# Performance work log

Measured on AMD Instinct MI355X. Metric: run time of the kernel, lower is better.

The kernel has to match this reference:

```python
import jax, jax.numpy as jnp
import numpy as np

TAU = 0.3  # default tau in selectCom_adap
K = 1      # hard-coded K in selectCom_adap

B, C, N, M = 8, 64, 2048, 2048


def setup_inputs() -> dict:
    key = jax.random.key(0)
    k1, k2, k3, k4 = jax.random.split(key, 4)
    return {
        "src_emb": jax.random.normal(k1, (B, C, N), dtype=jnp.float32),
        "tgt_emb": jax.random.normal(k2, (B, C, M), dtype=jnp.float32),
        "src": jax.random.normal(k3, (B, 3, N), dtype=jnp.float32),
        "tgt": jax.random.normal(k4, (B, 3, M), dtype=jnp.float32),
    }


def reference(src_emb, tgt_emb, src, tgt):
    # EPCOR eval path: selectCom_adap + get_sparse_w
    dtype = src_emb.dtype
    Np = src_emb.shape[2]
    Mp = tgt_emb.shape[2]
    tgt_K = int(Mp * TAU)
    src_K = int(Np * TAU)

    inner = jnp.einsum('bcn,bcm->bnm', src_emb, tgt_emb)
    xx = jnp.sum(src_emb * src_emb, axis=1)[:, :, None]   # [B,N,1]
    yy = jnp.sum(tgt_emb * tgt_emb, axis=1)[:, None, :]   # [B,1,M]
    pd = 2.0 * inner - xx - yy                             # [B,N,M]

    # column softmax and tgt outlier mask (smallest tgt_K column mass)
    scoresSoftCol = jax.nn.softmax(pd, axis=2)
    scoresColSum = jnp.sum(scoresSoftCol, axis=1)          # [B,M]
    col_thresh = -jax.lax.top_k(-scoresColSum, tgt_K)[0][:, -1]  # tgt_K-th smallest, [B]
    mask_tgt = (scoresColSum < col_thresh[:, None])[:, None, :]  # [B,1,M]

    # row softmax and src outlier mask (smallest src_K row mass)
    scoresSoftRow = jax.nn.softmax(pd, axis=1)
    scoresRowSum = jnp.sum(scoresSoftRow, axis=2)          # [B,N]
    row_thresh = -jax.lax.top_k(-scoresRowSum, src_K)[0][:, -1]  # [B]
    mask_src = (scoresRowSum < row_thresh[:, None])[:, :, None]  # [B,N,1]

    mask = jnp.logical_or(mask_src, mask_tgt)              # [B,N,M]

    # torch precedence: mask = (mask + scoresSoftCol) < topk  (bool promoted to float)
    topk = jax.lax.top_k(scoresSoftCol, K)[0][..., -1:]    # K-th largest per row, [B,N,1]
    mask = (mask.astype(dtype) + scoresSoftCol) < topk     # [B,N,M]

    w_sparse = jnp.where(mask, jnp.zeros((), dtype), scoresSoftCol)
    colsum = jnp.sum(w_sparse, axis=-1, keepdims=True)
    colsum = jnp.where(colsum < 1e-5, jnp.asarray(1e-5, dtype), colsum)
    src_tgt_weight = w_sparse / colsum                     # row-renormalized sparse weights

    val_sum = jnp.sum(src_tgt_weight, axis=-1, keepdims=True)  # [B,N,1]
    val_sum_inlier = jnp.where(mask_src, jnp.zeros((), dtype), val_sum)[..., 0]  # [B,N]
    src_weight = val_sum_inlier / jnp.sum(val_sum_inlier, axis=-1, keepdims=True)

    # src_corr = tgt @ src_tgt_weight^T : [B,3,M] x [B,N,M] -> [B,3,N]
    src_corr = jnp.einsum('bdm,bnm->bdn', tgt, src_tgt_weight)
    return src_corr, src_weight, mask_src, mask_tgt
```

## Files before the change

### kernel.cpp

```cpp
#include <hip/hip_runtime.h>

#define BB 8
#define CC 64
#define NN 2048
#define MM 2048
#define KSEL 613
#define MT 32
#define MT2 16
#define NT2 16
#define NCH 16

#define OUT_W  (BB * 3 * NN)
#define OUT_MS (OUT_W + BB * NN)
#define OUT_MT (OUT_MS + BB * NN)

typedef __bf16 bf16x8 __attribute__((ext_vector_type(8)));
typedef float f32x4 __attribute__((ext_vector_type(4)));

__global__ __launch_bounds__(256) void sqnorm_k(const float* __restrict__ E,
                                                float* __restrict__ out, int L) {
    int b = blockIdx.y;
    int i = blockIdx.x * 256 + threadIdx.x;
    const float* p = E + (size_t)b * CC * L + i;
    float s = 0.f;
#pragma unroll
    for (int c = 0; c < CC; ++c) { float v = p[(size_t)c * L]; s += v * v; }
    out[b * L + i] = s;
}

__device__ __forceinline__ void build3(const float* sm, int base,
                                       bf16x8& v0, bf16x8& v1, bf16x8& v2) {
#pragma unroll
    for (int j = 0; j < 8; ++j) {
        float a = sm[base + (j << 7)];
        __bf16 h0 = (__bf16)a;
        float f0 = (float)h0;
        float r1 = a - f0;
        __bf16 h1 = (__bf16)r1;
        float f1 = (float)h1;
        float r2 = r1 - f1;
        __bf16 h2 = (__bf16)r2;
        v0[j] = h0; v1[j] = h1; v2[j] = h2;
    }
}

#define GLD_LDS16(gsrc, ldst)                                                        \
    __builtin_amdgcn_global_load_lds(                                                \
        (const __attribute__((address_space(1))) void*)(gsrc),                       \
        (__attribute__((address_space(3))) void*)(ldst), 16, 0, 0)

__global__ __launch_bounds__(256, 2) void gemm_pd_k(const float* __restrict__ A,
                                                    const float* __restrict__ Bm,
                                                    const float* __restrict__ xx,
                                                    const float* __restrict__ yy,
                                                    float* __restrict__ pd,
                                                    float* __restrict__ rpM,
                                                    float* __restrict__ rpS,
                                                    float* __restrict__ cpM,
                                                    float* __restrict__ cpS) {
    __shared__ float As[CC * 128];
    __shared__ float Bs[CC * 128];
    __shared__ float rowm2[2][128], rows2[2][128];
    __shared__ float colm2[2][128], cols2[2][128];
    int b = blockIdx.z;
    int n0 = blockIdx.y << 7;
    int m0 = blockIdx.x << 7;
    int t = threadIdx.x;

    const float* Ab = A + (size_t)b * CC * NN + n0;
    const float* Bb = Bm + (size_t)b * CC * MM + m0;
#pragma unroll
    for (int i = 0; i < 8; ++i) {
        int fi = i * 256 + t;
        int c = fi >> 5, nb = fi & 31;
        GLD_LDS16(Ab + (size_t)c * NN + nb * 4, As + fi * 4);
        GLD_LDS16(Bb + (size_t)c * MM + nb * 4, Bs + fi * 4);
    }
    __syncthreads();

    int lane = t & 63, w = t >> 6;
    int wn = w >> 1, wm = w & 1;
    int g = lane >> 4, q = lane & 15;

    f32x4 acc[4][4] = {};

#pragma unroll
    for (int kc = 0; kc < 2; ++kc) {
        bf16x8 a0[4], a1[4], a2[4];
#pragma unroll
        for (int ng = 0; ng < 4; ++ng)
            build3(As, (kc * 32 + g * 8) * 128 + wn * 64 + ng * 16 + q,
                   a0[ng], a1[ng], a2[ng]);
#pragma unroll
        for (int mg = 0; mg < 4; ++mg) {
            bf16x8 b0, b1, b2;
            build3(Bs, (kc * 32 + g * 8) * 128 + wm * 64 + mg * 16 + q, b0, b1, b2);
#pragma unroll
            for (int ng = 0; ng < 4; ++ng)
                acc[ng][mg] = __builtin_amdgcn_mfma_f32_16x16x32_bf16(a0[ng], b0, acc[ng][mg], 0, 0, 0);
#pragma unroll
            for (int ng = 0; ng < 4; ++ng)
                acc[ng][mg] = __builtin_amdgcn_mfma_f32_16x16x32_bf16(a0[ng], b1, acc[ng][mg], 0, 0, 0);
#pragma unroll
            for (int ng = 0; ng < 4; ++ng)
                acc[ng][mg] = __builtin_amdgcn_mfma_f32_16x16x32_bf16(a1[ng], b0, acc[ng][mg], 0, 0, 0);
#pragma unroll
            for (int ng = 0; ng < 4; ++ng)
                acc[ng][mg] = __builtin_amdgcn_mfma_f32_16x16x32_bf16(a1[ng], b1, acc[ng][mg], 0, 0, 0);
#pragma unroll
            for (int ng = 0; ng < 4; ++ng)
                acc[ng][mg] = __builtin_amdgcn_mfma_f32_16x16x32_bf16(a0[ng], b2, acc[ng][mg], 0, 0, 0);
#pragma unroll
            for (int ng = 0; ng < 4; ++ng)
                acc[ng][mg] = __builtin_amdgcn_mfma_f32_16x16x32_bf16(a2[ng], b0, acc[ng][mg], 0, 0, 0);
        }
    }

    int nbase = n0 + wn * 64;
    int mbase = m0 + wm * 64;
    float xv[4][4];
#pragma unroll
    for (int ng = 0; ng < 4; ++ng)
#pragma unroll
        for (int r = 0; r < 4; ++r)
            xv[ng][r] = xx[b * NN + nbase + ng * 16 + g * 4 + r];
    float yv[4];
#pragma unroll
    for (int mg = 0; mg < 4; ++mg) yv[mg] = yy[b * MM + mbase + mg * 16 + q];

#pragma unroll
    for (int ng = 0; ng < 4; ++ng)
#pragma unroll
        for (int r = 0; r < 4; ++r) {
            float* prow = pd + ((size_t)(b * NN + nbase + ng * 16 + g * 4 + r)) * MM + mbase + q;
#pragma unroll
            for (int mg = 0; mg < 4; ++mg) {
                float o = 2.f * acc[ng][mg][r] - xv[ng][r] - yv[mg];
                acc[ng][mg][r] = o;
                prow[mg * 16] = o;
            }
        }

#pragma unroll
    for (int ng = 0; ng < 4; ++ng)
#pragma unroll
        for (int r = 0; r < 4; ++r) {
            float mx = fmaxf(fmaxf(acc[ng][0][r], acc[ng][1][r]),
                             fmaxf(acc[ng][2][r], acc[ng][3][r]));
#pragma unroll
            for (int d = 1; d < 16; d <<= 1) mx = fmaxf(mx, __shfl_xor(mx, d));
            float s = __expf(acc[ng][0][r] - mx) + __expf(acc[ng][1][r] - mx) +
                      __expf(acc[ng][2][r] - mx) + __expf(acc[ng][3][r] - mx);
#pragma unroll
            for (int d = 1; d < 16; d <<= 1) s += __shfl_xor(s, d);
            if (q == 0) {
                int nl = wn * 64 + ng * 16 + g * 4 + r;
                rowm2[wm][nl] = mx;
                rows2[wm][nl] = s;
            }
        }

#pragma unroll
    for (int mg = 0; mg < 4; ++mg) {
        float cx = -3.4e38f;
#pragma unroll
        for (int ng = 0; ng < 4; ++ng)
#pragma unroll
            for (int r = 0; r < 4; ++r) cx = fmaxf(cx, acc[ng][mg][r]);
        cx = fmaxf(cx, __shfl_xor(cx, 16));
        cx = fmaxf(cx, __shfl_xor(cx, 32));
        float cs = 0.f;
#pragma unroll
        for (int ng = 0; ng < 4; ++ng)
#pragma unroll
            for (int r = 0; r < 4; ++r) cs += __expf(acc[ng][mg][r] - cx);
        cs += __shfl_xor(cs, 16);
        cs += __shfl_xor(cs, 32);
        if (lane < 16) {
            int ml = wm * 64 + mg * 16 + q;
            colm2[wn][ml] = cx;
            cols2[wn][ml] = cs;
        }
    }
    __syncthreads();

    if (t < 128) {
        float ma = rowm2[0][t], mb = rowm2[1][t];
        float M = fmaxf(ma, mb);
        float S = rows2[0][t] * __expf(ma - M) + rows2[1][t] * __expf(mb - M);
        size_t base = ((size_t)(b * MT2 + blockIdx.x)) * NN + n0 + t;
        rpM[base] = M;
        rpS[base] = S;
    } else {
        int m = t - 128;
        float ma = colm2[0][m], mb = colm2[1][m];
        float M = fmaxf(ma, mb);
        float S = cols2[0][m] * __expf(ma - M) + cols2[1][m] * __expf(mb - M);
        size_t base = ((size_t)(b * NT2 + blockIdx.y)) * MM + m0 + m;
        cpM[base] = M;
        cpS[base] = S;
    }
}

__global__ __launch_bounds__(256) void comb_rc_k(const float* __restrict__ rpM,
                                                 const float* __restrict__ rpS,
                                                 const float* __restrict__ cpM,
                                                 const float* __restrict__ cpS,
                                                 float* __restrict__ rowmax,
                                                 float* __restrict__ rowsum,
                                                 float* __restrict__ colmax,
                                                 float* __restrict__ colsum) {
    int b = blockIdx.y, which = blockIdx.z;
    int i = blockIdx.x * 256 + threadIdx.x;
    const float* pM = which ? cpM : rpM;
    const float* pS = which ? cpS : rpS;
    float* oM = which ? colmax : rowmax;
    float* oS = which ? colsum : rowsum;
    float Mv = -3.4e38f;
#pragma unroll
    for (int k = 0; k < 16; ++k) Mv = fmaxf(Mv, pM[(size_t)(b * 16 + k) * 2048 + i]);
    float S = 0.f;
#pragma unroll
    for (int k = 0; k < 16; ++k) {
        size_t o = (size_t)(b * 16 + k) * 2048 + i;
        S += pS[o] * __expf(pM[o] - Mv);
    }
    oM[b * 2048 + i] = Mv;
    oS[b * 2048 + i] = S;
}

__global__ __launch_bounds__(256) void cross_k(const float* __restrict__ pd,
                                               const float* __restrict__ rowmax,
                                               const float* __restrict__ rowsum,
                                               const float* __restrict__ colmax,
                                               const float* __restrict__ colsum,
                                               float* __restrict__ sRowp,
                                               float* __restrict__ sColp) {
    __shared__ float rmx[128], rin[128];
    __shared__ float rowpart[128][65];
    __shared__ float colacc[4][64];
    int b = blockIdx.z, nc = blockIdx.y, mtile = blockIdx.x;
    int m0 = mtile << 6;
    int t = threadIdx.x, mL = t & 63, ng = t >> 6;
    if (t < 128) {
        int n = nc * 128 + t;
        rmx[t] = rowmax[b * NN + n];
        rin[t] = 1.f / rowsum[b * NN + n];
    }
    float cmv = colmax[b * MM + m0 + mL];
    float civ = 1.f / colsum[b * MM + m0 + mL];
    __syncthreads();
    const float* base = pd + ((size_t)(b * NN + nc * 128)) * MM + m0 + mL;
    float scp = 0.f;
#pragma unroll
    for (int i = 0; i < 32; ++i) {
        int nl = (i << 2) + ng;
        float v = base[(size_t)nl * MM];
        scp += __expf(v - rmx[nl]) * rin[nl];
        rowpart[nl][mL] = __expf(v - cmv) * civ;
    }
    colacc[ng][mL] = scp;
    __syncthreads();
    if (t < 128) {
        float s = 0.f;
#pragma unroll
        for (int c = 0; c < 64; ++c) s += rowpart[t][c];
        sRowp[((size_t)(b * MT + mtile)) * NN + nc * 128 + t] = s;
    } else if (t < 192) {
        int m = t - 128;
        sColp[((size_t)(b * NCH + nc)) * MM + m0 + m] =
            colacc[0][m] + colacc[1][m] + colacc[2][m] + colacc[3][m];
    }
}

__global__ __launch_bounds__(256) void comb_s_k(const float* __restrict__ sRowp,
                                                const float* __restrict__ sColp,
                                                float* __restrict__ sRow,
                                                float* __restrict__ sCol) {
    int b = blockIdx.y, which = blockIdx.z;
    int i = blockIdx.x * 256 + threadIdx.x;
    if (!which) {
        float s = 0.f;
#pragma unroll
        for (int k = 0; k < MT; ++k) s += sRowp[(size_t)(b * MT + k) * NN + i];
        sRow[b * NN + i] = s;
    } else {
        float s = 0.f;
#pragma unroll
        for (int k = 0; k < NCH; ++k) s += sColp[(size_t)(b * NCH + k) * MM + i];
        sCol[b * MM + i] = s;
    }
}

__global__ __launch_bounds__(64) void select_k(const float* __restrict__ sRow,
                                               const float* __restrict__ sCol,
                                               float* __restrict__ rth,
                                               float* __restrict__ cth) {
    int kind = blockIdx.x, b = blockIdx.y, t = threadIdx.x;
    const float* vals = (kind == 0) ? (sRow + b * NN) : (sCol + b * MM);
    float v[32];
#pragma unroll
    for (int i = 0; i < 32; ++i) v[i] = vals[t + (i << 6)];
    unsigned lo = 0u, hi = 0x7F800000u;
    while (lo < hi) {
        unsigned mid = lo + ((hi - lo) >> 1);
        float pv = __uint_as_float(mid);
        int c = 0;
#pragma unroll
        for (int i = 0; i < 32; ++i) c += (v[i] <= pv) ? 1 : 0;
#pragma unroll
        for (int off = 32; off > 0; off >>= 1) c += __shfl_down(c, off);
        c = __shfl(c, 0);
        if (c >= KSEL + 1) hi = mid; else lo = mid + 1;
    }
    if (t == 0) { if (kind == 0) rth[b] = __uint_as_float(lo); else cth[b] = __uint_as_float(lo); }
}

__global__ __launch_bounds__(256) void masks_k(const float* __restrict__ sRow,
                                               const float* __restrict__ sCol,
                                               const float* __restrict__ rth,
                                               const float* __restrict__ cth,
                                               float* __restrict__ out) {
    int b = blockIdx.x, t = threadIdx.x;
    float r = rth[b], c = cth[b];
    int cnt = 0;
    bool ms[8];
#pragma unroll
    for (int i = 0; i < 8; ++i) {
        int n = t + (i << 8);
        ms[i] = sRow[b * NN + n] < r;
        out[OUT_MS + b * NN + n] = ms[i] ? 1.f : 0.f;
        out[OUT_MT + b * MM + n] = (sCol[b * MM + n] < c) ? 1.f : 0.f;
        cnt += ms[i] ? 0 : 1;
    }
#pragma unroll
    for (int off = 32; off > 0; off >>= 1) cnt += __shfl_down(cnt, off);
    __shared__ int wcnt[4];
    int wave = t >> 6, lane = t & 63;
    if (lane == 0) wcnt[wave] = cnt;
    __syncthreads();
    float inv = 1.f / (float)(wcnt[0] + wcnt[1] + wcnt[2] + wcnt[3]);
#pragma unroll
    for (int i = 0; i < 8; ++i) {
        int n = t + (i << 8);
        out[OUT_W + b * NN + n] = ms[i] ? 0.f : inv;
    }
}

__global__ __launch_bounds__(256) void corr_k(const float* __restrict__ pd,
                                              const float* __restrict__ rowmax,
                                              const float* __restrict__ rowsum,
                                              const float* __restrict__ sRow,
                                              const float* __restrict__ sCol,
                                              const float* __restrict__ rth,
                                              const float* __restrict__ cth,
                                              const float* __restrict__ tgt,
                                              float* __restrict__ out) {
    int b = blockIdx.y, n = blockIdx.x, t = threadIdx.x;
    const float4* row4 = (const float4*)(pd + ((size_t)b * NN + n) * MM);
    const float4* sc4 = (const float4*)(sCol + b * MM);
    const float4* tg4 = (const float4*)(tgt + (size_t)b * 3 * MM);
    float rmax = rowmax[b * NN + n];
    float rsum = rowsum[b * NN + n];
    float cthv = cth[b];
    bool msrc = sRow[b * NN + n] < rth[b];
    float cs = 0.f, d0 = 0.f, d1 = 0.f, d2 = 0.f;
#pragma unroll
    for (int g = 0; g < 2; ++g) {
        int j = t + (g << 8);
        float p[4], sc[4], t0[4], t1[4], t2[4];
        *(float4*)p = row4[j];
        *(float4*)sc = sc4[j];
        *(float4*)t0 = tg4[j];
        *(float4*)t1 = tg4[j + MM / 4];
        *(float4*)t2 = tg4[j + MM / 2];
#pragma unroll
        for (int c = 0; c < 4; ++c) {
            bool keep = msrc || (sc[c] < cthv) || (p[c] == rmax);
            if (keep) {
                float s = __expf(p[c] - rmax) / rsum;
                cs += s;
                d0 += s * t0[c];
                d1 += s * t1[c];
                d2 += s * t2[c];
            }
        }
    }
#pragma unroll
    for (int off = 32; off > 0; off >>= 1) {
        cs += __shfl_down(cs, off);
        d0 += __shfl_down(d0, off);
        d1 += __shfl_down(d1, off);
        d2 += __shfl_down(d2, off);
    }
    __shared__ float red[4][4];
    int wave = t >> 6, lane = t & 63;
    if (lane == 0) { red[wave][0] = cs; red[wave][1] = d0; red[wave][2] = d1; red[wave][3] = d2; }
    __syncthreads();
    if (t == 0) {
        float cT = red[0][0] + red[1][0] + red[2][0] + red[3][0];
        float e0 = red[0][1] + red[1][1] + red[2][1] + red[3][1];
        float e1 = red[0][2] + red[1][2] + red[2][2] + red[3][2];
        float e2 = red[0][3] + red[1][3] + red[2][3] + red[3][3];
        cT = (cT < 1e-5f) ? 1e-5f : cT;
        out[(b * 3 + 0) * NN + n] = e0 / cT;
        out[(b * 3 + 1) * NN + n] = e1 / cT;
        out[(b * 3 + 2) * NN + n] = e2 / cT;
    }
}

extern "C" void kernel_launch(void* const* d_in, const int* in_sizes, int n_in,
                              void* d_out, int out_size, void* d_ws, size_t ws_size,
                              hipStream_t stream) {
    const float* src_emb = (const float*)d_in[0];
    const float* tgt_emb = (const float*)d_in[1];
    const float* tgt = (const float*)d_in[3];
    float* out = (float*)d_out;

    float* ws = (float*)d_ws;
    float* pd     = ws;
    float* xx     = pd + (size_t)BB * NN * MM;
    float* yy     = xx + BB * NN;
    float* rowmax = yy + BB * MM;
    float* rowsum = rowmax + BB * NN;
    float* colmax = rowsum + BB * NN;
    float* colsum = colmax + BB * MM;
    float* sRow   = colsum + BB * MM;
    float* sCol   = sRow + BB * NN;
    float* rth    = sCol + BB * MM;
    float* cth    = rth + BB;
    float* rpM    = cth + BB;
    float* rpS    = rpM + (size_t)BB * MT * NN;
    float* cpM    = rpS + (size_t)BB * MT * NN;
    float* cpS    = cpM + (size_t)BB * MT * MM;
    float* sRowp  = cpS + (size_t)BB * MT * MM;
    float* sColp  = sRowp + (size_t)BB * MT * NN;

    sqnorm_k<<<dim3(NN / 256, BB), 256, 0, stream>>>(src_emb, xx, NN);
    sqnorm_k<<<dim3(MM / 256, BB), 256, 0, stream>>>(tgt_emb, yy, MM);
    gemm_pd_k<<<dim3(MM / 128, NN / 128, BB), 256, 0, stream>>>(src_emb, tgt_emb, xx, yy, pd,
                                                                rpM, rpS, cpM, cpS);
    comb_rc_k<<<dim3(2048 / 256, BB, 2), 256, 0, stream>>>(rpM, rpS, cpM, cpS,
                                                           rowmax, rowsum, colmax, colsum);
    cross_k<<<dim3(MT, NCH, BB), 256, 0, stream>>>(pd, rowmax, rowsum, colmax, colsum, sRowp, sColp);
    comb_s_k<<<dim3(2048 / 256, BB, 2), 256, 0, stream>>>(sRowp, sColp, sRow, sCol);
    select_k<<<dim3(2, BB), 64, 0, stream>>>(sRow, sCol, rth, cth);
    masks_k<<<dim3(BB), 256, 0, stream>>>(sRow, sCol, rth, cth, out);
    corr_k<<<dim3(NN, BB), 256, 0, stream>>>(pd, rowmax, rowsum, sRow, sCol, rth, cth, tgt, out);
}
```

Before: 242.4 us.

## Pre-split embeddings into bf16 triples and stage swizzled tiles in GEMM

A new split_k kernel computes the squared norms and splits each embedding value into three bf16 parts once, writing them transposed and packed in pairs. The GEMM then loads these pre-split tiles into LDS with XOR swizzling and reads the MFMA fragments directly, instead of converting fp32 to bf16 triples inside every block. This removes conversion work that was repeated across blocks and cuts LDS use, which allows 3 blocks per SM. In exchange it adds extra global traffic for the split arrays and more barriers inside the k loop. The workspace layout for the partial buffers is also changed.

```diff
diff --git a/kernel.cpp b/kernel.cpp
--- a/kernel.cpp
+++ b/kernel.cpp
@@ -16,104 +16,152 @@
 
 typedef __bf16 bf16x8 __attribute__((ext_vector_type(8)));
 typedef float f32x4 __attribute__((ext_vector_type(4)));
-
-__global__ __launch_bounds__(256) void sqnorm_k(const float* __restrict__ E,
-                                                float* __restrict__ out, int L) {
-    int b = blockIdx.y;
-    int i = blockIdx.x * 256 + threadIdx.x;
-    const float* p = E + (size_t)b * CC * L + i;
-    float s = 0.f;
-#pragma unroll
-    for (int c = 0; c < CC; ++c) { float v = p[(size_t)c * L]; s += v * v; }
-    out[b * L + i] = s;
-}
-
-__device__ __forceinline__ void build3(const float* sm, int base,
-                                       bf16x8& v0, bf16x8& v1, bf16x8& v2) {
-#pragma unroll
-    for (int j = 0; j < 8; ++j) {
-        float a = sm[base + (j << 7)];
-        __bf16 h0 = (__bf16)a;
-        float f0 = (float)h0;
-        float r1 = a - f0;
-        __bf16 h1 = (__bf16)r1;
-        float f1 = (float)h1;
-        float r2 = r1 - f1;
-        __bf16 h2 = (__bf16)r2;
-        v0[j] = h0; v1[j] = h1; v2[j] = h2;
-    }
-}
-
-#define GLD_LDS16(gsrc, ldst)                                                        \
-    __builtin_amdgcn_global_load_lds(                                                \
-        (const __attribute__((address_space(1))) void*)(gsrc),                       \
-        (__attribute__((address_space(3))) void*)(ldst), 16, 0, 0)
-
-__global__ __launch_bounds__(256, 2) void gemm_pd_k(const float* __restrict__ A,
-                                                    const float* __restrict__ Bm,
-                                                    const float* __restrict__ xx,
-                                                    const float* __restrict__ yy,
-                                                    float* __restrict__ pd,
-                                                    float* __restrict__ rpM,
-                                                    float* __restrict__ rpS,
-                                                    float* __restrict__ cpM,
-                                                    float* __restrict__ cpS) {
-    __shared__ float As[CC * 128];
-    __shared__ float Bs[CC * 128];
+typedef unsigned short u16;
+
+#define MFMA16 __builtin_amdgcn_mfma_f32_16x16x32_bf16
+
+__device__ __forceinline__ void split3(float a, u16& u0, u16& u1, u16& u2) {
+    __bf16 h0 = (__bf16)a; float f0 = (float)h0;
+    float r1 = a - f0;
+    __bf16 h1 = (__bf16)r1; float f1 = (float)h1;
+    float r2 = r1 - f1;
+    __bf16 h2 = (__bf16)r2;
+    u0 = __builtin_bit_cast(u16, h0);
+    u1 = __builtin_bit_cast(u16, h1);
+    u2 = __builtin_bit_cast(u16, h2);
+}
+
+__global__ __launch_bounds__(256) void split_k(const float* __restrict__ E,
+                                               float* __restrict__ sq,
+                                               unsigned* __restrict__ T0,
+                                               unsigned* __restrict__ T1,
+                                               unsigned* __restrict__ T2) {
+    __shared__ float Ls[64][65];
+    __shared__ float sacc[64];
+    int b = blockIdx.y, n0 = blockIdx.x * 64, t = threadIdx.x;
+    const float* Eb = E + (size_t)b * CC * NN + n0;
+#pragma unroll
+    for (int i = 0; i < 4; ++i) {
+        int idx = (i << 8) + t, c = idx >> 4, nq = idx & 15;
+        float4 v = *(const float4*)(Eb + (size_t)c * NN + (nq << 2));
+        Ls[c][nq * 4 + 0] = v.x; Ls[c][nq * 4 + 1] = v.y;
+        Ls[c][nq * 4 + 2] = v.z; Ls[c][nq * 4 + 3] = v.w;
+    }
+    __syncthreads();
+    int j = t & 31, nn = t >> 5;
+#pragma unroll
+    for (int p = 0; p < 8; ++p) {
+        int n = (p << 3) + nn;
+        float a = Ls[2 * j][n], c = Ls[2 * j + 1][n];
+        float s = a * a + c * c;
+#pragma unroll
+        for (int d = 1; d < 32; d <<= 1) s += __shfl_xor(s, d);
+        if (j == 0) sacc[n] = s;
+        u16 a0, a1, a2, c0, c1, c2;
+        split3(a, a0, a1, a2);
+        split3(c, c0, c1, c2);
+        size_t row = (size_t)(b * NN + n0 + n) * 32 + j;
+        T0[row] = (unsigned)a0 | ((unsigned)c0 << 16);
+        T1[row] = (unsigned)a1 | ((unsigned)c1 << 16);
+        T2[row] = (unsigned)a2 | ((unsigned)c2 << 16);
+    }
+    __syncthreads();
+    if (t < 64) sq[b * NN + n0 + t] = sacc[t];
+}
+
+__device__ __forceinline__ void stage_tile(u16* dst, const unsigned* src,
+                                           int base_nm, int kc, int t) {
+#pragma unroll
+    for (int i = 0; i < 2; ++i) {
+        int d = (((i << 8) + t) << 4);
+        int nn_ = d >> 6, c4 = (d >> 4) & 3;
+        const char* gs = (const char*)src + ((size_t)(base_nm + nn_) << 7) +
+                         ((size_t)kc << 6) + ((c4 ^ (nn_ & 3)) << 4);
+        __builtin_amdgcn_global_load_lds(
+            (const __attribute__((address_space(1))) void*)gs,
+            (__attribute__((address_space(3))) void*)((char*)dst + d), 16, 0, 0);
+    }
+}
+
+__device__ __forceinline__ bf16x8 frag(const u16* tile, int nloc, int g) {
+    return *(const bf16x8*)((const char*)tile + (nloc << 6) + ((g ^ (nloc & 3)) << 4));
+}
+
+__global__ __launch_bounds__(256, 3) void gemm_pd_k(
+    const unsigned* __restrict__ A0, const unsigned* __restrict__ A1, const unsigned* __restrict__ A2,
+    const unsigned* __restrict__ B0, const unsigned* __restrict__ B1, const unsigned* __restrict__ B2,
+    const float* __restrict__ xx, const float* __restrict__ yy,
+    float* __restrict__ pd,
+    float* __restrict__ rpM, float* __restrict__ rpS,
+    float* __restrict__ cpM, float* __restrict__ cpS) {
+    __shared__ u16 Ta0[128 * 32], Tb0[128 * 32], Tax[128 * 32], Tbx[128 * 32];
     __shared__ float rowm2[2][128], rows2[2][128];
     __shared__ float colm2[2][128], cols2[2][128];
     int b = blockIdx.z;
     int n0 = blockIdx.y << 7;
     int m0 = blockIdx.x << 7;
-    int t = threadIdx.x;
-
-    const float* Ab = A + (size_t)b * CC * NN + n0;
-    const float* Bb = Bm + (size_t)b * CC * MM + m0;
-#pragma unroll
-    for (int i = 0; i < 8; ++i) {
-        int fi = i * 256 + t;
-        int c = fi >> 5, nb = fi & 31;
-        GLD_LDS16(Ab + (size_t)c * NN + nb * 4, As + fi * 4);
-        GLD_LDS16(Bb + (size_t)c * MM + nb * 4, Bs + fi * 4);
-    }
-    __syncthreads();
-
-    int lane = t & 63, w = t >> 6;
+    int t = threadIdx.x, lane = t & 63, w = t >> 6;
     int wn = w >> 1, wm = w & 1;
     int g = lane >> 4, q = lane & 15;
+    int baseA = b * NN + n0, baseB = b * MM + m0;
 
     f32x4 acc[4][4] = {};
 
 #pragma unroll
     for (int kc = 0; kc < 2; ++kc) {
-        bf16x8 a0[4], a1[4], a2[4];
-#pragma unroll
-        for (int ng = 0; ng < 4; ++ng)
-            build3(As, (kc * 32 + g * 8) * 128 + wn * 64 + ng * 16 + q,
-                   a0[ng], a1[ng], a2[ng]);
-#pragma unroll
-        for (int mg = 0; mg < 4; ++mg) {
-            bf16x8 b0, b1, b2;
-            build3(Bs, (kc * 32 + g * 8) * 128 + wm * 64 + mg * 16 + q, b0, b1, b2);
+        stage_tile(Ta0, A0, baseA, kc, t);
+        stage_tile(Tb0, B0, baseB, kc, t);
+        stage_tile(Tax, A1, baseA, kc, t);
+        stage_tile(Tbx, B1, baseB, kc, t);
+        __syncthreads();
+        bf16x8 fa0[4], fb0[4], fax[4], fbx[4];
+#pragma unroll
+        for (int i = 0; i < 4; ++i) {
+            fa0[i] = frag(Ta0, wn * 64 + i * 16 + q, g);
+            fb0[i] = frag(Tb0, wm * 64 + i * 16 + q, g);
+            fax[i] = frag(Tax, wn * 64 + i * 16 + q, g);
+            fbx[i] = frag(Tbx, wm * 64 + i * 16 + q, g);
+        }
+#pragma unroll
+        for (int mg = 0; mg < 4; ++mg)
 #pragma unroll
             for (int ng = 0; ng < 4; ++ng)
-                acc[ng][mg] = __builtin_amdgcn_mfma_f32_16x16x32_bf16(a0[ng], b0, acc[ng][mg], 0, 0, 0);
+                acc[ng][mg] = MFMA16(fa0[ng], fb0[mg], acc[ng][mg], 0, 0, 0);
+#pragma unroll
+        for (int mg = 0; mg < 4; ++mg)
 #pragma unroll
             for (int ng = 0; ng < 4; ++ng)
-                acc[ng][mg] = __builtin_amdgcn_mfma_f32_16x16x32_bf16(a0[ng], b1, acc[ng][mg], 0, 0, 0);
+                acc[ng][mg] = MFMA16(fa0[ng], fbx[mg], acc[ng][mg], 0, 0, 0);
+#pragma unroll
+        for (int mg = 0; mg < 4; ++mg)
 #pragma unroll
             for (int ng = 0; ng < 4; ++ng)
-                acc[ng][mg] = __builtin_amdgcn_mfma_f32_16x16x32_bf16(a1[ng], b0, acc[ng][mg], 0, 0, 0);
+                acc[ng][mg] = MFMA16(fax[ng], fb0[mg], acc[ng][mg], 0, 0, 0);
+#pragma unroll
+        for (int mg = 0; mg < 4; ++mg)
 #pragma unroll
             for (int ng = 0; ng < 4; ++ng)
-                acc[ng][mg] = __builtin_amdgcn_mfma_f32_16x16x32_bf16(a1[ng], b1, acc[ng][mg], 0, 0, 0);
+                acc[ng][mg] = MFMA16(fax[ng], fbx[mg], acc[ng][mg], 0, 0, 0);
+        __syncthreads();
+        stage_tile(Tax, A2, baseA, kc, t);
+        stage_tile(Tbx, B2, baseB, kc, t);
+        __syncthreads();
+#pragma unroll
+        for (int i = 0; i < 4; ++i) {
+            fax[i] = frag(Tax, wn * 64 + i * 16 + q, g);
+            fbx[i] = frag(Tbx, wm * 64 + i * 16 + q, g);
+        }
+#pragma unroll
+        for (int mg = 0; mg < 4; ++mg)
 #pragma unroll
             for (int ng = 0; ng < 4; ++ng)
-                acc[ng][mg] = __builtin_amdgcn_mfma_f32_16x16x32_bf16(a0[ng], b2, acc[ng][mg], 0, 0, 0);
+                acc[ng][mg] = MFMA16(fa0[ng], fbx[mg], acc[ng][mg], 0, 0, 0);
+#pragma unroll
+        for (int mg = 0; mg < 4; ++mg)
 #pragma unroll
             for (int ng = 0; ng < 4; ++ng)
-                acc[ng][mg] = __builtin_amdgcn_mfma_f32_16x16x32_bf16(a2[ng], b0, acc[ng][mg], 0, 0, 0);
-        }
+                acc[ng][mg] = MFMA16(fax[ng], fb0[mg], acc[ng][mg], 0, 0, 0);
+        __syncthreads();
     }
 
     int nbase = n0 + wn * 64;
@@ -430,16 +478,22 @@
     float* rth    = sCol + BB * MM;
     float* cth    = rth + BB;
     float* rpM    = cth + BB;
-    float* rpS    = rpM + (size_t)BB * MT * NN;
-    float* cpM    = rpS + (size_t)BB * MT * NN;
-    float* cpS    = cpM + (size_t)BB * MT * MM;
-    float* sRowp  = cpS + (size_t)BB * MT * MM;
+    float* rpS    = rpM + (size_t)BB * 16 * NN;
+    float* cpM    = rpS + (size_t)BB * 16 * NN;
+    float* cpS    = cpM + (size_t)BB * 16 * MM;
+    float* sRowp  = cpS + (size_t)BB * 16 * MM;
     float* sColp  = sRowp + (size_t)BB * MT * NN;
-
-    sqnorm_k<<<dim3(NN / 256, BB), 256, 0, stream>>>(src_emb, xx, NN);
-    sqnorm_k<<<dim3(MM / 256, BB), 256, 0, stream>>>(tgt_emb, yy, MM);
-    gemm_pd_k<<<dim3(MM / 128, NN / 128, BB), 256, 0, stream>>>(src_emb, tgt_emb, xx, yy, pd,
-                                                                rpM, rpS, cpM, cpS);
+    unsigned* At0 = (unsigned*)(sColp + (size_t)BB * NCH * MM);
+    unsigned* At1 = At0 + (size_t)BB * NN * 32;
+    unsigned* At2 = At1 + (size_t)BB * NN * 32;
+    unsigned* Bt0 = At2 + (size_t)BB * NN * 32;
+    unsigned* Bt1 = Bt0 + (size_t)BB * MM * 32;
+    unsigned* Bt2 = Bt1 + (size_t)BB * MM * 32;
+
+    split_k<<<dim3(NN / 64, BB), 256, 0, stream>>>(src_emb, xx, At0, At1, At2);
+    split_k<<<dim3(MM / 64, BB), 256, 0, stream>>>(tgt_emb, yy, Bt0, Bt1, Bt2);
+    gemm_pd_k<<<dim3(MM / 128, NN / 128, BB), 256, 0, stream>>>(At0, At1, At2, Bt0, Bt1, Bt2,
+                                                                xx, yy, pd, rpM, rpS, cpM, cpS);
     comb_rc_k<<<dim3(2048 / 256, BB, 2), 256, 0, stream>>>(rpM, rpS, cpM, cpS,
                                                            rowmax, rowsum, colmax, colsum);
     cross_k<<<dim3(MT, NCH, BB), 256, 0, stream>>>(pd, rowmax, rowsum, colmax, colsum, sRowp, sColp);
```

After: 203.4 us. 16.1% less time.
